# Kernel optimization log

Measured on AMD Instinct MI355X. Metric: run time of the kernel, lower is better.

## Reference

```python
import jax, jax.numpy as jnp
import numpy as np

NUM_CLUSTERS = 64  # label vocabulary size (labels in [0, NUM_CLUSTERS))


def setup_inputs() -> dict:
    key = jax.random.key(0)
    kf, kl = jax.random.split(key)
    features = jax.random.normal(kf, (8192, 128), dtype=jnp.float32)
    labels = jax.random.randint(kl, (8192,), 0, NUM_CLUSTERS, dtype=jnp.int64)
    return {"features": features, "labels": labels}


def _pairwise_dist(x):
    # Euclidean cdist with a grad-safe sqrt (zero entries -> zero, no NaN grads).
    sq = jnp.sum(x * x, axis=-1)                      # [N]
    d2 = sq[:, None] + sq[None, :] - 2.0 * (x @ x.T)  # [N, N]
    d2 = jnp.maximum(d2, 0.0)
    pos = d2 > 0
    return jnp.sqrt(jnp.where(pos, d2, 1.0)) * pos.astype(x.dtype)


def reference(features, labels):
    N = features.shape[0]
    C = NUM_CLUSTERS
    dtype = features.dtype

    onehot = jax.nn.one_hot(labels, C, dtype=dtype)   # [N, C]
    counts = jnp.sum(onehot, axis=0)                  # [C]

    dists = _pairwise_dist(features)                  # [N, N]
    # Per-sample sum of distances to each cluster: segment-sum over columns.
    S = dists @ onehot                                # [N, C]

    own_count = counts[labels]                        # [N]
    idx = jnp.arange(N)
    # mean intra-cluster distance a_i (exclude self: divide by n-1)
    a = S[idx, labels] / jnp.maximum(own_count - 1.0, 1.0)

    # mean distance to every other cluster; mask own cluster and empty clusters
    mean_inter = S / jnp.maximum(counts, 1.0)[None, :]          # [N, C]
    invalid = (onehot > 0) | (counts[None, :] == 0)
    big = jnp.asarray(jnp.finfo(dtype).max, dtype)
    b = jnp.min(jnp.where(invalid, big, mean_inter), axis=1)    # [N]

    score = (b - a) / jnp.maximum(b, a)
    # singleton clusters get score 0 (matches torch branch num_elements <= 1)
    score = jnp.where(own_count > 1, score, jnp.zeros((), dtype))
    return jnp.mean(score)
```

## Files before the change

kernel.cpp:

```cpp
#include <hip/hip_runtime.h>
#include <hip/hip_fp16.h>
#include <float.h>

#define NC 64
#define FD 128
#define LSTR 136

typedef _Float16 f16x8 __attribute__((ext_vector_type(8)));
typedef float f32x4 __attribute__((ext_vector_type(4)));

__global__ void prep_kernel(const float* __restrict__ feat,
                            const int* __restrict__ labels,
                            float* __restrict__ sq,
                            unsigned short* __restrict__ Xh,
                            unsigned short* __restrict__ Mt,
                            float* __restrict__ S,
                            float* __restrict__ out, int out_size,
                            int* __restrict__ counts, int N) {
  __shared__ int hist[NC];
  int t = threadIdx.x;
  if (t < NC) hist[t] = 0;
  __syncthreads();
  int row = blockIdx.x * 32 + (t >> 3);
  int o = t & 7;
  if (row < N) {
    const float* rp = feat + (size_t)row * FD;
    float s = 0.f;
#pragma unroll
    for (int j = 0; j < 4; ++j) {
      int c4 = o + 8 * j;
      float4 v = *(const float4*)(rp + c4 * 4);
      ushort4 h;
      h.x = __half_as_ushort(__float2half(v.x));
      h.y = __half_as_ushort(__float2half(v.y));
      h.z = __half_as_ushort(__float2half(v.z));
      h.w = __half_as_ushort(__float2half(v.w));
      *(ushort4*)&Xh[(size_t)row * FD + c4 * 4] = h;
      s = fmaf(v.x, v.x, s); s = fmaf(v.y, v.y, s);
      s = fmaf(v.z, v.z, s); s = fmaf(v.w, v.w, s);
    }
    s += __shfl_xor(s, 1); s += __shfl_xor(s, 2); s += __shfl_xor(s, 4);
    if (o == 0) { sq[row] = s; atomicAdd(&hist[labels[row]], 1); }
  }
  if ((blockIdx.x + 1) * 32 <= N) {
    float4 z = {0.f, 0.f, 0.f, 0.f};
    size_t base = (size_t)blockIdx.x * 32 * NC + t * 8;
    *(float4*)&S[base] = z;
    *(float4*)&S[base + 4] = z;
  }
  if (blockIdx.x == 0 && t < out_size) out[t] = 0.f;
  {
    int chunksPerN = N >> 3;
    int total = NC * chunksPerN;
    for (int id = blockIdx.x * 256 + t; id < total; id += gridDim.x * 256) {
      int n = id / chunksPerN;
      int c0 = (id - n * chunksPerN) * 8;
      ushort4 lo, hi;
      lo.x = (labels[c0 + 0] == n) ? 0x3C00 : 0;
      lo.y = (labels[c0 + 1] == n) ? 0x3C00 : 0;
      lo.z = (labels[c0 + 2] == n) ? 0x3C00 : 0;
      lo.w = (labels[c0 + 3] == n) ? 0x3C00 : 0;
      hi.x = (labels[c0 + 4] == n) ? 0x3C00 : 0;
      hi.y = (labels[c0 + 5] == n) ? 0x3C00 : 0;
      hi.z = (labels[c0 + 6] == n) ? 0x3C00 : 0;
      hi.w = (labels[c0 + 7] == n) ? 0x3C00 : 0;
      *(ushort4*)&Mt[(size_t)n * N + c0] = lo;
      *(ushort4*)&Mt[(size_t)n * N + c0 + 4] = hi;
    }
  }
  __syncthreads();
  if (t < NC) atomicAdd(&counts[t], hist[t]);
}

__global__ __launch_bounds__(256, 2)
void mfma_tile_kernel(const unsigned short* __restrict__ Xh,
                      const float* __restrict__ sq,
                      const unsigned short* __restrict__ Mt,
                      float* __restrict__ S,
                      int N, int colsPerSplit) {
  __shared__ __align__(16) unsigned short Ah[128 * LSTR];
  __shared__ __align__(16) unsigned short Bh[128 * LSTR];

  const int t = threadIdx.x;
  const int R = blockIdx.x * 128;
  const int cBeg = blockIdx.y * colsPerSplit;
  const int wave = t >> 6, lane = t & 63;
  const int mm = lane & 15, quad = lane >> 4;
  const int wr = wave >> 1, wc = wave & 1;

#pragma unroll
  for (int it = 0; it < 8; ++it) {
    int c = t + it * 256;
    int r = c >> 4, k0 = (c & 15) * 8;
    *(uint4*)&Ah[r * LSTR + k0] = *(const uint4*)&Xh[(size_t)(R + r) * FD + k0];
  }
  float sqi_r[4];
#pragma unroll
  for (int ib = 0; ib < 4; ++ib)
    sqi_r[ib] = sq[R + wr * 64 + ib * 16 + mm];

  f32x4 sacc[2][4];
#pragma unroll
  for (int rt = 0; rt < 2; ++rt)
#pragma unroll
    for (int lt = 0; lt < 4; ++lt) sacc[rt][lt] = (f32x4)0.f;

  const int numTiles = colsPerSplit / 128;
  for (int ct = 0; ct < numTiles; ++ct) {
    const int C0 = cBeg + ct * 128;
    __syncthreads();
#pragma unroll
    for (int it = 0; it < 8; ++it) {
      int c = t + it * 256;
      int r = c >> 4, k0 = (c & 15) * 8;
      *(uint4*)&Bh[r * LSTR + k0] = *(const uint4*)&Xh[(size_t)(C0 + r) * FD + k0];
    }
    float sjr[4][4];
#pragma unroll
    for (int jb = 0; jb < 4; ++jb)
#pragma unroll
      for (int r = 0; r < 4; ++r)
        sjr[jb][r] = sq[C0 + wc * 64 + jb * 16 + quad * 4 + r];
    __syncthreads();

    f32x4 dacc[4][4];
#pragma unroll
    for (int ib = 0; ib < 4; ++ib)
#pragma unroll
      for (int jb = 0; jb < 4; ++jb) dacc[ib][jb] = (f32x4)0.f;

#pragma unroll
    for (int ks = 0; ks < 4; ++ks) {
      const int ko = ks * 32 + quad * 8;
      f16x8 af[4], bf[4];
#pragma unroll
      for (int ib = 0; ib < 4; ++ib)
        af[ib] = *(const f16x8*)&Ah[(wr * 64 + ib * 16 + mm) * LSTR + ko];
#pragma unroll
      for (int jb = 0; jb < 4; ++jb)
        bf[jb] = *(const f16x8*)&Bh[(wc * 64 + jb * 16 + mm) * LSTR + ko];
#pragma unroll
      for (int ib = 0; ib < 4; ++ib)
#pragma unroll
        for (int jb = 0; jb < 4; ++jb)
          dacc[ib][jb] = __builtin_amdgcn_mfma_f32_16x16x32_f16(bf[jb], af[ib], dacc[ib][jb], 0, 0, 0);
    }
    __syncthreads();

    const bool hasDiag = (R == C0);
#pragma unroll
    for (int ib = 0; ib < 4; ++ib) {
      const int rowLocal = wr * 64 + ib * 16 + mm;
      const float si = sqi_r[ib];
#pragma unroll
      for (int jb = 0; jb < 4; ++jb) {
        const int colBase = wc * 64 + jb * 16 + quad * 4;
        float d[4];
#pragma unroll
        for (int r = 0; r < 4; ++r) {
          float d2 = fmaf(-2.f, dacc[ib][jb][r], si + sjr[jb][r]);
          d[r] = __builtin_amdgcn_sqrtf(fmaxf(d2, 0.f));
        }
        if (hasDiag) {
#pragma unroll
          for (int r = 0; r < 4; ++r)
            if (rowLocal == colBase + r) d[r] = 0.f;
        }
        uint2 pk;
        pk.x = __builtin_bit_cast(unsigned, __builtin_amdgcn_cvt_pkrtz(d[0], d[1]));
        pk.y = __builtin_bit_cast(unsigned, __builtin_amdgcn_cvt_pkrtz(d[2], d[3]));
        *(uint2*)&Bh[rowLocal * LSTR + colBase] = pk;
      }
    }
    __syncthreads();

#pragma unroll
    for (int ks = 0; ks < 4; ++ks) {
      const int ko = ks * 32 + quad * 8;
      f16x8 da0 = *(const f16x8*)&Bh[(wave * 32 + mm) * LSTR + ko];
      f16x8 da1 = *(const f16x8*)&Bh[(wave * 32 + 16 + mm) * LSTR + ko];
#pragma unroll
      for (int lt = 0; lt < 4; ++lt) {
        f16x8 mb = *(const f16x8*)&Mt[(size_t)(lt * 16 + mm) * N + C0 + ks * 32 + quad * 8];
        sacc[0][lt] = __builtin_amdgcn_mfma_f32_16x16x32_f16(da0, mb, sacc[0][lt], 0, 0, 0);
        sacc[1][lt] = __builtin_amdgcn_mfma_f32_16x16x32_f16(da1, mb, sacc[1][lt], 0, 0, 0);
      }
    }
  }

#pragma unroll
  for (int rt = 0; rt < 2; ++rt)
#pragma unroll
    for (int lt = 0; lt < 4; ++lt)
#pragma unroll
      for (int r = 0; r < 4; ++r) {
        int row = wave * 32 + rt * 16 + quad * 4 + r;
        atomicAdd(&S[(size_t)(R + row) * NC + lt * 16 + mm], sacc[rt][lt][r]);
      }
}

__global__ void score_kernel(const float* __restrict__ S,
                             const int* __restrict__ labels,
                             const int* __restrict__ counts,
                             float* __restrict__ out, int N) {
  __shared__ float cnt_s[NC];
  __shared__ float inv_s[NC];
  __shared__ float red[128];
  int t = threadIdx.x;
  if (t < NC) {
    float c = (float)counts[t];
    cnt_s[t] = c;
    inv_s[t] = 1.f / fmaxf(c, 1.f);
  }
  __syncthreads();
  int i = blockIdx.x * 128 + t;
  float score = 0.f;
  if (i < N) {
    int li = labels[i];
    float own = cnt_s[li];
    const float4* Sv = (const float4*)(S + (size_t)i * NC);
    float a = S[(size_t)i * NC + li] / fmaxf(own - 1.f, 1.f);
    float b = FLT_MAX;
#pragma unroll
    for (int c4 = 0; c4 < NC / 4; ++c4) {
      float4 v = Sv[c4];
      int c = c4 * 4;
      float m0 = v.x * inv_s[c + 0];
      float m1 = v.y * inv_s[c + 1];
      float m2 = v.z * inv_s[c + 2];
      float m3 = v.w * inv_s[c + 3];
      b = fminf(b, (c + 0 == li || cnt_s[c + 0] == 0.f) ? FLT_MAX : m0);
      b = fminf(b, (c + 1 == li || cnt_s[c + 1] == 0.f) ? FLT_MAX : m1);
      b = fminf(b, (c + 2 == li || cnt_s[c + 2] == 0.f) ? FLT_MAX : m2);
      b = fminf(b, (c + 3 == li || cnt_s[c + 3] == 0.f) ? FLT_MAX : m3);
    }
    float mx = fmaxf(a, b);
    score = (own > 1.f) ? (b - a) / mx : 0.f;
  }
  red[t] = score;
  __syncthreads();
  for (int sft = 64; sft > 0; sft >>= 1) {
    if (t < sft) red[t] += red[t + sft];
    __syncthreads();
  }
  if (t == 0) atomicAdd(out, red[0] / (float)N);
}

extern "C" void kernel_launch(void* const* d_in, const int* in_sizes, int n_in,
                              void* d_out, int out_size, void* d_ws, size_t ws_size,
                              hipStream_t stream) {
  const float* feat = (const float*)d_in[0];
  const int* labels = (const int*)d_in[1];
  const int N = in_sizes[1];
  float* out = (float*)d_out;
  char* ws = (char*)d_ws;

  int*   counts = (int*)ws;
  float* sq     = (float*)(ws + 256);
  size_t o = 256 + (size_t)N * 4;
  o = (o + 255) & ~(size_t)255;
  unsigned short* Xh = (unsigned short*)(ws + o);
  unsigned short* Mt = (unsigned short*)(ws + o + (size_t)N * FD * 2);
  float* S = (float*)(ws + o + (size_t)N * FD * 2 + (size_t)NC * N * 2);

  (void)hipMemsetAsync(counts, 0, 256, stream);

  prep_kernel<<<(N + 31) / 32, 256, 0, stream>>>(feat, labels, sq, Xh, Mt, S,
                                                 out, out_size, counts, N);

  const int colSplit = 8;
  dim3 grid(N / 128, colSplit);
  mfma_tile_kernel<<<grid, 256, 0, stream>>>(Xh, sq, Mt, S, N, N / colSplit);

  score_kernel<<<(N + 127) / 128, 128, 0, stream>>>(S, labels, counts, out, N);
}
```

Before: 126.0 us.

## Keep A fragments in registers and prefetch next B tile via registers

The A row-block fragments are loaded once into registers, which frees the A shared buffer to serve as the distance staging buffer. The next column tile of X is prefetched from global memory into registers while the current tile is processed, then written to shared memory after the segment-sum MFMAs. This cuts the number of barriers per tile from four to two and hides global load latency. The cost is higher register pressure (16 f16x8 A fragments plus 8 uint4 prefetch registers), which could cause spills or limit occupancy under launch_bounds(256,2).

```diff
diff --git a/kernel.cpp b/kernel.cpp
--- a/kernel.cpp
+++ b/kernel.cpp
@@ -78,8 +78,8 @@
                       const unsigned short* __restrict__ Mt,
                       float* __restrict__ S,
                       int N, int colsPerSplit) {
-  __shared__ __align__(16) unsigned short Ah[128 * LSTR];
-  __shared__ __align__(16) unsigned short Bh[128 * LSTR];
+  __shared__ __align__(16) unsigned short bufA[128 * LSTR];
+  __shared__ __align__(16) unsigned short bufB[128 * LSTR];
 
   const int t = threadIdx.x;
   const int R = blockIdx.x * 128;
@@ -87,41 +87,61 @@
   const int wave = t >> 6, lane = t & 63;
   const int mm = lane & 15, quad = lane >> 4;
   const int wr = wave >> 1, wc = wave & 1;
-
+  const int numTiles = colsPerSplit / 128;
+
+  const int sr = t >> 4;
+  const int sk = (t & 15) * 8;
+
+  uint4 areg[8], breg[8];
 #pragma unroll
   for (int it = 0; it < 8; ++it) {
-    int c = t + it * 256;
-    int r = c >> 4, k0 = (c & 15) * 8;
-    *(uint4*)&Ah[r * LSTR + k0] = *(const uint4*)&Xh[(size_t)(R + r) * FD + k0];
+    int r = sr + it * 16;
+    areg[it] = *(const uint4*)&Xh[(size_t)(R + r) * FD + sk];
+    breg[it] = *(const uint4*)&Xh[(size_t)(cBeg + r) * FD + sk];
+  }
+#pragma unroll
+  for (int it = 0; it < 8; ++it) {
+    int r = sr + it * 16;
+    *(uint4*)&bufA[r * LSTR + sk] = areg[it];
+    *(uint4*)&bufB[r * LSTR + sk] = breg[it];
+  }
+  __syncthreads();
+
+  f16x8 af[4][4];
+#pragma unroll
+  for (int ks = 0; ks < 4; ++ks) {
+    const int ko = ks * 32 + quad * 8;
+#pragma unroll
+    for (int ib = 0; ib < 4; ++ib)
+      af[ib][ks] = *(const f16x8*)&bufA[(wr * 64 + ib * 16 + mm) * LSTR + ko];
   }
   float sqi_r[4];
 #pragma unroll
   for (int ib = 0; ib < 4; ++ib)
     sqi_r[ib] = sq[R + wr * 64 + ib * 16 + mm];
 
+  if (numTiles > 1) {
+#pragma unroll
+    for (int it = 0; it < 8; ++it)
+      breg[it] = *(const uint4*)&Xh[(size_t)(cBeg + 128 + sr + it * 16) * FD + sk];
+  }
+
   f32x4 sacc[2][4];
 #pragma unroll
   for (int rt = 0; rt < 2; ++rt)
 #pragma unroll
     for (int lt = 0; lt < 4; ++lt) sacc[rt][lt] = (f32x4)0.f;
 
-  const int numTiles = colsPerSplit / 128;
+  __syncthreads();
+
   for (int ct = 0; ct < numTiles; ++ct) {
     const int C0 = cBeg + ct * 128;
-    __syncthreads();
-#pragma unroll
-    for (int it = 0; it < 8; ++it) {
-      int c = t + it * 256;
-      int r = c >> 4, k0 = (c & 15) * 8;
-      *(uint4*)&Bh[r * LSTR + k0] = *(const uint4*)&Xh[(size_t)(C0 + r) * FD + k0];
-    }
     float sjr[4][4];
 #pragma unroll
     for (int jb = 0; jb < 4; ++jb)
 #pragma unroll
       for (int r = 0; r < 4; ++r)
         sjr[jb][r] = sq[C0 + wc * 64 + jb * 16 + quad * 4 + r];
-    __syncthreads();
 
     f32x4 dacc[4][4];
 #pragma unroll
@@ -132,20 +152,16 @@
 #pragma unroll
     for (int ks = 0; ks < 4; ++ks) {
       const int ko = ks * 32 + quad * 8;
-      f16x8 af[4], bf[4];
+      f16x8 bf[4];
+#pragma unroll
+      for (int jb = 0; jb < 4; ++jb)
+        bf[jb] = *(const f16x8*)&bufB[(wc * 64 + jb * 16 + mm) * LSTR + ko];
 #pragma unroll
       for (int ib = 0; ib < 4; ++ib)
-        af[ib] = *(const f16x8*)&Ah[(wr * 64 + ib * 16 + mm) * LSTR + ko];
-#pragma unroll
-      for (int jb = 0; jb < 4; ++jb)
-        bf[jb] = *(const f16x8*)&Bh[(wc * 64 + jb * 16 + mm) * LSTR + ko];
-#pragma unroll
-      for (int ib = 0; ib < 4; ++ib)
 #pragma unroll
         for (int jb = 0; jb < 4; ++jb)
-          dacc[ib][jb] = __builtin_amdgcn_mfma_f32_16x16x32_f16(bf[jb], af[ib], dacc[ib][jb], 0, 0, 0);
-    }
-    __syncthreads();
+          dacc[ib][jb] = __builtin_amdgcn_mfma_f32_16x16x32_f16(bf[jb], af[ib][ks], dacc[ib][jb], 0, 0, 0);
+    }
 
     const bool hasDiag = (R == C0);
 #pragma unroll
@@ -169,7 +185,7 @@
         uint2 pk;
         pk.x = __builtin_bit_cast(unsigned, __builtin_amdgcn_cvt_pkrtz(d[0], d[1]));
         pk.y = __builtin_bit_cast(unsigned, __builtin_amdgcn_cvt_pkrtz(d[2], d[3]));
-        *(uint2*)&Bh[rowLocal * LSTR + colBase] = pk;
+        *(uint2*)&bufA[rowLocal * LSTR + colBase] = pk;
       }
     }
     __syncthreads();
@@ -177,8 +193,8 @@
 #pragma unroll
     for (int ks = 0; ks < 4; ++ks) {
       const int ko = ks * 32 + quad * 8;
-      f16x8 da0 = *(const f16x8*)&Bh[(wave * 32 + mm) * LSTR + ko];
-      f16x8 da1 = *(const f16x8*)&Bh[(wave * 32 + 16 + mm) * LSTR + ko];
+      f16x8 da0 = *(const f16x8*)&bufA[(wave * 32 + mm) * LSTR + ko];
+      f16x8 da1 = *(const f16x8*)&bufA[(wave * 32 + 16 + mm) * LSTR + ko];
 #pragma unroll
       for (int lt = 0; lt < 4; ++lt) {
         f16x8 mb = *(const f16x8*)&Mt[(size_t)(lt * 16 + mm) * N + C0 + ks * 32 + quad * 8];
@@ -186,6 +202,18 @@
         sacc[1][lt] = __builtin_amdgcn_mfma_f32_16x16x32_f16(da1, mb, sacc[1][lt], 0, 0, 0);
       }
     }
+
+    if (ct + 1 < numTiles) {
+#pragma unroll
+      for (int it = 0; it < 8; ++it)
+        *(uint4*)&bufB[(sr + it * 16) * LSTR + sk] = breg[it];
+      if (ct + 2 < numTiles) {
+#pragma unroll
+        for (int it = 0; it < 8; ++it)
+          breg[it] = *(const uint4*)&Xh[(size_t)(C0 + 256 + sr + it * 16) * FD + sk];
+      }
+    }
+    __syncthreads();
   }
 
 #pragma unroll
```

New measurement: 149.7 us. 1.19x slower.

## Use 8 waves per tile block and register-prefetch next B tile

Applied to the files above, without the earlier changes.

Doubles the block to 512 threads (8 waves), so each wave computes a 64x32 slice of the distance tile and a 16-row slice of the cluster sums. Register pressure per wave drops and more waves are available to hide latency. The next column tile of features is loaded from global memory into registers while the current tile is computed, then written into shared memory after the segment-sum MFMAs. This adds an extra barrier per tile and raises the occupancy request to 4 blocks per CU, which could force register spills.

```diff
diff --git a/kernel.cpp b/kernel.cpp
--- a/kernel.cpp
+++ b/kernel.cpp
@@ -72,7 +72,7 @@
   if (t < NC) atomicAdd(&counts[t], hist[t]);
 }
 
-__global__ __launch_bounds__(256, 2)
+__global__ __launch_bounds__(512, 4)
 void mfma_tile_kernel(const unsigned short* __restrict__ Xh,
                       const float* __restrict__ sq,
                       const unsigned short* __restrict__ Mt,
@@ -86,63 +86,75 @@
   const int cBeg = blockIdx.y * colsPerSplit;
   const int wave = t >> 6, lane = t & 63;
   const int mm = lane & 15, quad = lane >> 4;
-  const int wr = wave >> 1, wc = wave & 1;
-
-#pragma unroll
-  for (int it = 0; it < 8; ++it) {
-    int c = t + it * 256;
-    int r = c >> 4, k0 = (c & 15) * 8;
-    *(uint4*)&Ah[r * LSTR + k0] = *(const uint4*)&Xh[(size_t)(R + r) * FD + k0];
-  }
+  const int wr = wave >> 2, wc = wave & 3;
+  const int numTiles = colsPerSplit / 128;
+
+  const int sr = t >> 4;
+  const int sk = (t & 15) * 8;
+
+  {
+    uint4 areg[4], b0[4];
+#pragma unroll
+    for (int it = 0; it < 4; ++it) {
+      int r = sr + it * 32;
+      areg[it] = *(const uint4*)&Xh[(size_t)(R + r) * FD + sk];
+      b0[it]   = *(const uint4*)&Xh[(size_t)(cBeg + r) * FD + sk];
+    }
+#pragma unroll
+    for (int it = 0; it < 4; ++it) {
+      int r = sr + it * 32;
+      *(uint4*)&Ah[r * LSTR + sk] = areg[it];
+      *(uint4*)&Bh[r * LSTR + sk] = b0[it];
+    }
+  }
+
   float sqi_r[4];
 #pragma unroll
   for (int ib = 0; ib < 4; ++ib)
     sqi_r[ib] = sq[R + wr * 64 + ib * 16 + mm];
 
-  f32x4 sacc[2][4];
-#pragma unroll
-  for (int rt = 0; rt < 2; ++rt)
-#pragma unroll
-    for (int lt = 0; lt < 4; ++lt) sacc[rt][lt] = (f32x4)0.f;
-
-  const int numTiles = colsPerSplit / 128;
+  uint4 breg[4];
+  if (numTiles > 1) {
+#pragma unroll
+    for (int it = 0; it < 4; ++it)
+      breg[it] = *(const uint4*)&Xh[(size_t)(cBeg + 128 + sr + it * 32) * FD + sk];
+  }
+
+  f32x4 sacc[4];
+#pragma unroll
+  for (int lt = 0; lt < 4; ++lt) sacc[lt] = (f32x4)0.f;
+
+  __syncthreads();
+
   for (int ct = 0; ct < numTiles; ++ct) {
     const int C0 = cBeg + ct * 128;
-    __syncthreads();
-#pragma unroll
-    for (int it = 0; it < 8; ++it) {
-      int c = t + it * 256;
-      int r = c >> 4, k0 = (c & 15) * 8;
-      *(uint4*)&Bh[r * LSTR + k0] = *(const uint4*)&Xh[(size_t)(C0 + r) * FD + k0];
-    }
-    float sjr[4][4];
-#pragma unroll
-    for (int jb = 0; jb < 4; ++jb)
+    float sjr[2][4];
+#pragma unroll
+    for (int jb = 0; jb < 2; ++jb)
 #pragma unroll
       for (int r = 0; r < 4; ++r)
-        sjr[jb][r] = sq[C0 + wc * 64 + jb * 16 + quad * 4 + r];
-    __syncthreads();
-
-    f32x4 dacc[4][4];
+        sjr[jb][r] = sq[C0 + wc * 32 + jb * 16 + quad * 4 + r];
+
+    f32x4 dacc[4][2];
 #pragma unroll
     for (int ib = 0; ib < 4; ++ib)
 #pragma unroll
-      for (int jb = 0; jb < 4; ++jb) dacc[ib][jb] = (f32x4)0.f;
+      for (int jb = 0; jb < 2; ++jb) dacc[ib][jb] = (f32x4)0.f;
 
 #pragma unroll
     for (int ks = 0; ks < 4; ++ks) {
       const int ko = ks * 32 + quad * 8;
-      f16x8 af[4], bf[4];
+      f16x8 af[4], bf[2];
 #pragma unroll
       for (int ib = 0; ib < 4; ++ib)
         af[ib] = *(const f16x8*)&Ah[(wr * 64 + ib * 16 + mm) * LSTR + ko];
 #pragma unroll
-      for (int jb = 0; jb < 4; ++jb)
-        bf[jb] = *(const f16x8*)&Bh[(wc * 64 + jb * 16 + mm) * LSTR + ko];
+      for (int jb = 0; jb < 2; ++jb)
+        bf[jb] = *(const f16x8*)&Bh[(wc * 32 + jb * 16 + mm) * LSTR + ko];
 #pragma unroll
       for (int ib = 0; ib < 4; ++ib)
 #pragma unroll
-        for (int jb = 0; jb < 4; ++jb)
+        for (int jb = 0; jb < 2; ++jb)
           dacc[ib][jb] = __builtin_amdgcn_mfma_f32_16x16x32_f16(bf[jb], af[ib], dacc[ib][jb], 0, 0, 0);
     }
     __syncthreads();
@@ -153,8 +165,8 @@
       const int rowLocal = wr * 64 + ib * 16 + mm;
       const float si = sqi_r[ib];
 #pragma unroll
-      for (int jb = 0; jb < 4; ++jb) {
-        const int colBase = wc * 64 + jb * 16 + quad * 4;
+      for (int jb = 0; jb < 2; ++jb) {
+        const int colBase = wc * 32 + jb * 16 + quad * 4;
         float d[4];
 #pragma unroll
         for (int r = 0; r < 4; ++r) {
@@ -177,26 +189,35 @@
 #pragma unroll
     for (int ks = 0; ks < 4; ++ks) {
       const int ko = ks * 32 + quad * 8;
-      f16x8 da0 = *(const f16x8*)&Bh[(wave * 32 + mm) * LSTR + ko];
-      f16x8 da1 = *(const f16x8*)&Bh[(wave * 32 + 16 + mm) * LSTR + ko];
+      f16x8 da = *(const f16x8*)&Bh[(wave * 16 + mm) * LSTR + ko];
 #pragma unroll
       for (int lt = 0; lt < 4; ++lt) {
         f16x8 mb = *(const f16x8*)&Mt[(size_t)(lt * 16 + mm) * N + C0 + ks * 32 + quad * 8];
-        sacc[0][lt] = __builtin_amdgcn_mfma_f32_16x16x32_f16(da0, mb, sacc[0][lt], 0, 0, 0);
-        sacc[1][lt] = __builtin_amdgcn_mfma_f32_16x16x32_f16(da1, mb, sacc[1][lt], 0, 0, 0);
+        sacc[lt] = __builtin_amdgcn_mfma_f32_16x16x32_f16(da, mb, sacc[lt], 0, 0, 0);
       }
     }
-  }
-
-#pragma unroll
-  for (int rt = 0; rt < 2; ++rt)
-#pragma unroll
-    for (int lt = 0; lt < 4; ++lt)
-#pragma unroll
-      for (int r = 0; r < 4; ++r) {
-        int row = wave * 32 + rt * 16 + quad * 4 + r;
-        atomicAdd(&S[(size_t)(R + row) * NC + lt * 16 + mm], sacc[rt][lt][r]);
+    __syncthreads();
+
+    if (ct + 1 < numTiles) {
+#pragma unroll
+      for (int it = 0; it < 4; ++it)
+        *(uint4*)&Bh[(sr + it * 32) * LSTR + sk] = breg[it];
+      if (ct + 2 < numTiles) {
+#pragma unroll
+        for (int it = 0; it < 4; ++it)
+          breg[it] = *(const uint4*)&Xh[(size_t)(C0 + 256 + sr + it * 32) * FD + sk];
       }
+      __syncthreads();
+    }
+  }
+
+#pragma unroll
+  for (int lt = 0; lt < 4; ++lt)
+#pragma unroll
+    for (int r = 0; r < 4; ++r) {
+      int row = wave * 16 + quad * 4 + r;
+      atomicAdd(&S[(size_t)(R + row) * NC + lt * 16 + mm], sacc[lt][r]);
+    }
 }
 
 __global__ void score_kernel(const float* __restrict__ S,
@@ -270,7 +291,7 @@
 
   const int colSplit = 8;
   dim3 grid(N / 128, colSplit);
-  mfma_tile_kernel<<<grid, 256, 0, stream>>>(Xh, sq, Mt, S, N, N / colSplit);
+  mfma_tile_kernel<<<grid, 512, 0, stream>>>(Xh, sq, Mt, S, N, N / colSplit);
 
   score_kernel<<<(N + 127) / 128, 128, 0, stream>>>(S, labels, counts, out, N);
 }
```

Result: slower. 166.1 us (+31.8%).

## Feed distance MFMA outputs directly into segment-sum MFMA and double block to 512 threads

Applied to the files above, without the earlier changes.

The distance tile is no longer written to shared memory and re-read for the one-hot segment sum. Each wave converts its distance accumulator fragment to fp16 and uses it directly as an operand of a 16x16x16 MFMA against one-hot columns loaded from global memory. This removes a shared-memory round trip and two barriers per column tile. Block size grows to 512 threads so each wave owns a 32x64 subtile, which halves the accumulator registers per wave but needs more one-hot loads and smaller MFMAs.

```diff
diff --git a/kernel.cpp b/kernel.cpp
--- a/kernel.cpp
+++ b/kernel.cpp
@@ -7,6 +7,7 @@
 #define LSTR 136
 
 typedef _Float16 f16x8 __attribute__((ext_vector_type(8)));
+typedef _Float16 f16x4 __attribute__((ext_vector_type(4)));
 typedef float f32x4 __attribute__((ext_vector_type(4)));
 
 __global__ void prep_kernel(const float* __restrict__ feat,
@@ -72,7 +73,7 @@
   if (t < NC) atomicAdd(&counts[t], hist[t]);
 }
 
-__global__ __launch_bounds__(256, 2)
+__global__ __launch_bounds__(512, 2)
 void mfma_tile_kernel(const unsigned short* __restrict__ Xh,
                       const float* __restrict__ sq,
                       const unsigned short* __restrict__ Mt,
@@ -87,78 +88,82 @@
   const int wave = t >> 6, lane = t & 63;
   const int mm = lane & 15, quad = lane >> 4;
   const int wr = wave >> 1, wc = wave & 1;
-
-#pragma unroll
-  for (int it = 0; it < 8; ++it) {
-    int c = t + it * 256;
+  const int numTiles = colsPerSplit / 128;
+
+#pragma unroll
+  for (int it = 0; it < 4; ++it) {
+    int c = t + it * 512;
     int r = c >> 4, k0 = (c & 15) * 8;
     *(uint4*)&Ah[r * LSTR + k0] = *(const uint4*)&Xh[(size_t)(R + r) * FD + k0];
   }
-  float sqi_r[4];
-#pragma unroll
-  for (int ib = 0; ib < 4; ++ib)
-    sqi_r[ib] = sq[R + wr * 64 + ib * 16 + mm];
+
+  float sqi_r[2];
+#pragma unroll
+  for (int ib = 0; ib < 2; ++ib)
+    sqi_r[ib] = sq[R + wr * 32 + ib * 16 + mm];
 
   f32x4 sacc[2][4];
 #pragma unroll
-  for (int rt = 0; rt < 2; ++rt)
-#pragma unroll
-    for (int lt = 0; lt < 4; ++lt) sacc[rt][lt] = (f32x4)0.f;
-
-  const int numTiles = colsPerSplit / 128;
+  for (int ib = 0; ib < 2; ++ib)
+#pragma unroll
+    for (int lt = 0; lt < 4; ++lt) sacc[ib][lt] = (f32x4)0.f;
+
   for (int ct = 0; ct < numTiles; ++ct) {
     const int C0 = cBeg + ct * 128;
     __syncthreads();
 #pragma unroll
-    for (int it = 0; it < 8; ++it) {
-      int c = t + it * 256;
+    for (int it = 0; it < 4; ++it) {
+      int c = t + it * 512;
       int r = c >> 4, k0 = (c & 15) * 8;
       *(uint4*)&Bh[r * LSTR + k0] = *(const uint4*)&Xh[(size_t)(C0 + r) * FD + k0];
     }
-    float sjr[4][4];
+    float4 sjr[4];
 #pragma unroll
     for (int jb = 0; jb < 4; ++jb)
-#pragma unroll
-      for (int r = 0; r < 4; ++r)
-        sjr[jb][r] = sq[C0 + wc * 64 + jb * 16 + quad * 4 + r];
+      sjr[jb] = *(const float4*)&sq[C0 + wc * 64 + jb * 16 + quad * 4];
     __syncthreads();
 
-    f32x4 dacc[4][4];
-#pragma unroll
-    for (int ib = 0; ib < 4; ++ib)
+    f32x4 dacc[2][4];
+#pragma unroll
+    for (int ib = 0; ib < 2; ++ib)
 #pragma unroll
       for (int jb = 0; jb < 4; ++jb) dacc[ib][jb] = (f32x4)0.f;
 
 #pragma unroll
     for (int ks = 0; ks < 4; ++ks) {
       const int ko = ks * 32 + quad * 8;
-      f16x8 af[4], bf[4];
-#pragma unroll
-      for (int ib = 0; ib < 4; ++ib)
-        af[ib] = *(const f16x8*)&Ah[(wr * 64 + ib * 16 + mm) * LSTR + ko];
+      f16x8 af[2], bf[4];
+#pragma unroll
+      for (int ib = 0; ib < 2; ++ib)
+        af[ib] = *(const f16x8*)&Ah[(wr * 32 + ib * 16 + mm) * LSTR + ko];
 #pragma unroll
       for (int jb = 0; jb < 4; ++jb)
         bf[jb] = *(const f16x8*)&Bh[(wc * 64 + jb * 16 + mm) * LSTR + ko];
 #pragma unroll
-      for (int ib = 0; ib < 4; ++ib)
+      for (int ib = 0; ib < 2; ++ib)
 #pragma unroll
         for (int jb = 0; jb < 4; ++jb)
           dacc[ib][jb] = __builtin_amdgcn_mfma_f32_16x16x32_f16(bf[jb], af[ib], dacc[ib][jb], 0, 0, 0);
     }
-    __syncthreads();
 
     const bool hasDiag = (R == C0);
 #pragma unroll
-    for (int ib = 0; ib < 4; ++ib) {
-      const int rowLocal = wr * 64 + ib * 16 + mm;
-      const float si = sqi_r[ib];
-#pragma unroll
-      for (int jb = 0; jb < 4; ++jb) {
-        const int colBase = wc * 64 + jb * 16 + quad * 4;
+    for (int jb = 0; jb < 4; ++jb) {
+      const int colBase = wc * 64 + jb * 16 + quad * 4;
+      f16x4 mb[4];
+#pragma unroll
+      for (int lt = 0; lt < 4; ++lt)
+        mb[lt] = *(const f16x4*)&Mt[(size_t)(lt * 16 + mm) * N + C0 + colBase];
+#pragma unroll
+      for (int ib = 0; ib < 2; ++ib) {
+        const int rowLocal = wr * 32 + ib * 16 + mm;
+        const float si = sqi_r[ib];
         float d[4];
 #pragma unroll
         for (int r = 0; r < 4; ++r) {
-          float d2 = fmaf(-2.f, dacc[ib][jb][r], si + sjr[jb][r]);
+          float sj = (r == 0) ? sjr[jb].x : (r == 1) ? sjr[jb].y
+                   : (r == 2) ? sjr[jb].z : sjr[jb].w;
+          float d2 = fmaf(-2.f, dacc[ib][jb][r], si + sj);
           d[r] = __builtin_amdgcn_sqrtf(fmaxf(d2, 0.f));
         }
         if (hasDiag) {
@@ -169,33 +174,22 @@
         uint2 pk;
         pk.x = __builtin_bit_cast(unsigned, __builtin_amdgcn_cvt_pkrtz(d[0], d[1]));
         pk.y = __builtin_bit_cast(unsigned, __builtin_amdgcn_cvt_pkrtz(d[2], d[3]));
-        *(uint2*)&Bh[rowLocal * LSTR + colBase] = pk;
+        f16x4 da = __builtin_bit_cast(f16x4, pk);
+#pragma unroll
+        for (int lt = 0; lt < 4; ++lt)
+          sacc[ib][lt] = __builtin_amdgcn_mfma_f32_16x16x16f16(da, mb[lt], sacc[ib][lt], 0, 0, 0);
       }
     }
-    __syncthreads();
-
-#pragma unroll
-    for (int ks = 0; ks < 4; ++ks) {
-      const int ko = ks * 32 + quad * 8;
-      f16x8 da0 = *(const f16x8*)&Bh[(wave * 32 + mm) * LSTR + ko];
-      f16x8 da1 = *(const f16x8*)&Bh[(wave * 32 + 16 + mm) * LSTR + ko];
-#pragma unroll
-      for (int lt = 0; lt < 4; ++lt) {
-        f16x8 mb = *(const f16x8*)&Mt[(size_t)(lt * 16 + mm) * N + C0 + ks * 32 + quad * 8];
-        sacc[0][lt] = __builtin_amdgcn_mfma_f32_16x16x32_f16(da0, mb, sacc[0][lt], 0, 0, 0);
-        sacc[1][lt] = __builtin_amdgcn_mfma_f32_16x16x32_f16(da1, mb, sacc[1][lt], 0, 0, 0);
-      }
-    }
-  }
-
-#pragma unroll
-  for (int rt = 0; rt < 2; ++rt)
+  }
+
+#pragma unroll
+  for (int ib = 0; ib < 2; ++ib)
 #pragma unroll
     for (int lt = 0; lt < 4; ++lt)
 #pragma unroll
       for (int r = 0; r < 4; ++r) {
-        int row = wave * 32 + rt * 16 + quad * 4 + r;
-        atomicAdd(&S[(size_t)(R + row) * NC + lt * 16 + mm], sacc[rt][lt][r]);
+        int rowD = wr * 32 + ib * 16 + quad * 4 + r;
+        atomicAdd(&S[(size_t)(R + rowD) * NC + lt * 16 + mm], sacc[ib][lt][r]);
       }
 }
 
@@ -270,7 +264,7 @@
 
   const int colSplit = 8;
   dim3 grid(N / 128, colSplit);
-  mfma_tile_kernel<<<grid, 256, 0, stream>>>(Xh, sq, Mt, S, N, N / colSplit);
+  mfma_tile_kernel<<<grid, 512, 0, stream>>>(Xh, sq, Mt, S, N, N / colSplit);
 
   score_kernel<<<(N + 127) / 128, 128, 0, stream>>>(S, labels, counts, out, N);
 }
```

Measured after the change: 178.1 us. 41.3% more time.
